# Performance work log

Hardware: AMD Instinct MI355X
Metric: run time of the kernel (lower is better)

## Reference

```python
import jax, jax.numpy as jnp
import numpy as np
from jax import lax

# Multi-scale VAR tokenizer encode: per scale, bilinear-resize the residual latent,
# FSQ-quantize it (Cosmos DI16x16 quantizer, levels [8,8,8,5,5,5]), then subtract the
# upsampled ResidualBlock(conv3x3 -> GELU -> conv3x3) reconstruction from the latent.

RESOLUTIONS = [(1, 1), (2, 2), (4, 4), (6, 6), (8, 8), (10, 10), (12, 12), (16, 16)]
LEVELS = np.array([8.0, 8.0, 8.0, 5.0, 5.0, 5.0], dtype=np.float32)  # FSQ levels, 6 channels
C, HIDDEN = 6, 48  # channels, channels * expansion_factor(8)
FSQ_EPS = 1e-3


def _resize(x, hw):
    # matches torch F.interpolate(mode='bilinear', align_corners=False) (half-pixel, no antialias)
    b, c = x.shape[0], x.shape[1]
    return jax.image.resize(x, (b, c, hw[0], hw[1]), method='bilinear', antialias=False)


def _fsq_quantize(z):
    # z: [B, 6, H, W] float32 -> codes in [-1, 1] quantized to per-channel levels
    l = jnp.asarray(LEVELS).reshape(1, C, 1, 1)
    half_l = (l - 1.0) * (1.0 + FSQ_EPS) / 2.0
    offset = jnp.where(jnp.mod(l, 2.0) == 0.0, 0.5, 0.0)
    shift = jnp.arctanh(offset / half_l)
    bounded = jnp.tanh(z + shift) * half_l - offset
    quantized = bounded + lax.stop_gradient(jnp.round(bounded) - bounded)  # straight-through
    half_width = jnp.floor(l / 2.0)
    return quantized / half_width


def _conv3x3(x, w, b):
    y = lax.conv_general_dilated(x, w, window_strides=(1, 1), padding='SAME',
                                 dimension_numbers=('NCHW', 'OIHW', 'NCHW'))
    return y + b.reshape(1, -1, 1, 1)


def _residual_block(x, w1, b1, w2, b2):
    h = _conv3x3(x, w1, b1)
    h = jax.nn.gelu(h, approximate=False)  # nn.GELU default = exact erf
    return _conv3x3(h, w2, b2)


def setup_inputs() -> dict:
    key = jax.random.key(0)
    k0, k1, k2 = jax.random.split(key, 3)
    B = 2048
    n = len(RESOLUTIONS)
    latents = jax.random.normal(k0, (B, C, 16, 16), dtype=jnp.float32)
    w1 = jax.random.normal(k1, (n, HIDDEN, C, 3, 3), dtype=jnp.float32) * 0.05
    b1 = jnp.zeros((n, HIDDEN), dtype=jnp.float32)
    w2 = jax.random.normal(k2, (n, C, HIDDEN, 3, 3), dtype=jnp.float32) * 0.05
    b2 = jnp.zeros((n, C), dtype=jnp.float32)
    return {"latents": latents, "w1": w1, "b1": b1, "w2": w2, "b2": b2}


def reference(latents, w1, b1, w2, b2):
    f = latents
    full_hw = f.shape[-2:]
    tokens = []
    for i, (h, w) in enumerate(RESOLUTIONS):
        f_curr = _resize(f, (h, w))
        r = _fsq_quantize(f_curr)  # tup[1] of Cosmos FSQ quantizer: quantized codes
        tokens.append(r)
        if i < len(RESOLUTIONS) - 1:
            z = _residual_block(r, w1[i], b1[i], w2[i], b2[i])
            z = _resize(z, full_hw)
            f = f - z
    # concatenate per-scale tokens flattened over (C,H,W) -> [B, 6*(1+4+16+36+64+100+144+256)] = [B, 3726]
    return jnp.concatenate([t.reshape(t.shape[0], -1) for t in tokens], axis=-1)
```

## Files before the change

### kernel.cpp

```cpp
#include <hip/hip_runtime.h>
#include <math.h>

#define NTHREADS 256

__constant__ int c_RESA[8] = {1, 2, 4, 6, 8, 10, 12, 16};
__constant__ int c_OFF6[8] = {0, 6, 30, 126, 342, 726, 1326, 2190};
__constant__ unsigned c_MAGIC[8] = {1048576u, 524288u, 262144u, 174763u,
                                    131072u, 104858u, 87382u, 65536u};

__global__ void __launch_bounds__(256)
prep_w2t_kernel(const float* __restrict__ w2g, float* __restrict__ w2t) {
    int tid = blockIdx.x * blockDim.x + threadIdx.x;
    for (int i = tid; i < 8 * 2592; i += gridDim.x * blockDim.x) {
        int e  = i & 3;
        int r  = i >> 2;
        int co = r % 6;  r /= 6;
        int c4 = r % 12; r /= 12;
        int j  = r % 9;
        int s  = r / 9;
        int ci = c4 * 4 + e;
        w2t[i] = w2g[((size_t)(s * 6 + co) * 48 + ci) * 9 + j];
    }
}

__device__ __forceinline__ void mk_tap(int o, float invs, int insz,
                                       int* i0, int* i1, float* w0, float* w1) {
    float fy = __fsub_rn(__fmul_rn(__fadd_rn((float)o, 0.5f), invs), 0.5f);
    float fl = floorf(fy);
    int y0 = (int)fl;
    float k0 = __fsub_rn(1.0f, fabsf(__fsub_rn(fy, fl)));
    float k1 = __fsub_rn(1.0f, fabsf(__fsub_rn(fy, __fadd_rn(fl, 1.0f))));
    bool v0 = (y0 >= 0);
    bool v1 = (y0 + 1 <= insz - 1);
    k0 = v0 ? k0 : 0.0f;
    k1 = v1 ? k1 : 0.0f;
    float ssum = __fadd_rn(k0, k1);
    *w0 = __fdiv_rn(k0, ssum);
    *w1 = __fdiv_rn(k1, ssum);
    *i0 = v0 ? y0 : 0;
    *i1 = v1 ? (y0 + 1) : (insz - 1);
}

__device__ __forceinline__ float gelu_exact(float x) {
    return __fmul_rn(__fmul_rn(0.5f, x),
                     __fadd_rn(1.0f, erff(__fmul_rn(x, 0.70710678118654752440f))));
}

__global__ void __launch_bounds__(NTHREADS)
var_tokenizer_kernel(const float* __restrict__ latents,
                     const float* __restrict__ w1g, const float* __restrict__ b1g,
                     const float* __restrict__ w2t, const float* __restrict__ b2g,
                     float* __restrict__ out) {
    __shared__ float f_l[1536];
    __shared__ float r_pad[6 * 196];
    __shared__ __align__(16) float h4[12 * 196 * 4];
    __shared__ float z_l[6 * 144];
    __shared__ int   dti0[16]; __shared__ int dti1[16];
    __shared__ float dtw0[16]; __shared__ float dtw1[16];
    __shared__ int   uti0[16]; __shared__ int uti1[16];
    __shared__ float utw0[16]; __shared__ float utw1[16];

    const int item = blockIdx.x;
    const int tid  = threadIdx.x;
    const int wv   = __builtin_amdgcn_readfirstlane(tid >> 6);
    const int lane = tid & 63;

    const float* lat  = latents + (size_t)item * 1536;
    float*       outb = out + (size_t)item * 3726;

    for (int i = tid; i < 1536; i += NTHREADS) f_l[i] = lat[i];
    for (int i = tid; i < 6 * 196;      i += NTHREADS) r_pad[i] = 0.0f;
    for (int i = tid; i < 12 * 196 * 4; i += NTHREADS) h4[i] = 0.0f;

    const float HL8 = (8.0f - 1.0f) * (1.0f + 1.0e-3f) / 2.0f;
    const float HL5 = (5.0f - 1.0f) * (1.0f + 1.0e-3f) / 2.0f;
    const float SH8 = (float)atanh((double)(0.5f / HL8));

    __syncthreads();

    for (int s = 0; s < 8; ++s) {
        const int R  = c_RESA[s];
        const int HW = R * R;
        const unsigned M = c_MAGIC[s];
        const bool last = (s == 7);

        if (tid < R) {
            float invs = __fdiv_rn(1.0f, __fdiv_rn((float)R, 16.0f));
            mk_tap(tid, invs, 16, &dti0[tid], &dti1[tid], &dtw0[tid], &dtw1[tid]);
        } else if (tid >= 64 && tid < 80 && !last) {
            int o = tid - 64;
            float invs = __fdiv_rn(1.0f, __fdiv_rn(16.0f, (float)R));
            mk_tap(o, invs, R, &uti0[o], &uti1[o], &utw0[o], &utw1[o]);
        }
        __syncthreads();

        const int off = c_OFF6[s];
        #pragma unroll 2
        for (int t = tid; t < 6 * HW; t += NTHREADS) {
            int rest = (int)(((unsigned)t * M) >> 20);
            int ox   = t - rest * R;
            int c    = (int)(((unsigned)rest * M) >> 20);
            int oy   = rest - c * R;
            float v;
            if (last) {
                v = f_l[t];
            } else {
                int y0 = dti0[oy], y1 = dti1[oy], x0 = dti0[ox], x1 = dti1[ox];
                float wy0 = dtw0[oy], wy1 = dtw1[oy], wx0 = dtw0[ox], wx1 = dtw1[ox];
                const float* fc = f_l + c * 256;
                float a00 = fc[y0 * 16 + x0], a01 = fc[y0 * 16 + x1];
                float a10 = fc[y1 * 16 + x0], a11 = fc[y1 * 16 + x1];
                float t0 = __fadd_rn(__fmul_rn(wy0, a00), __fmul_rn(wy1, a10));
                float t1 = __fadd_rn(__fmul_rn(wy0, a01), __fmul_rn(wy1, a11));
                v = __fadd_rn(__fmul_rn(wx0, t0), __fmul_rn(wx1, t1));
            }
            bool is8 = (c < 3);
            float hl   = is8 ? HL8 : HL5;
            float offc = is8 ? 0.5f : 0.0f;
            float sh   = is8 ? SH8 : 0.0f;
            float arg  = __fadd_rn(v, sh);
            float th32 = tanhf(arg);
            float b32  = __fsub_rn(__fmul_rn(th32, hl), offc);
            float r32  = rintf(b32);
            float d    = __fsub_rn(b32, r32);
            if (fabsf(fabsf(d) - 0.5f) < 1e-4f) {
                float th = (float)tanh((double)arg);
                r32 = rintf(__fsub_rn(__fmul_rn(th, hl), offc));
            }
            float q = __fmul_rn(r32, is8 ? 0.25f : 0.5f);
            outb[off + t] = q;
            if (!last) r_pad[c * 196 + (oy + 1) * 14 + (ox + 1)] = q;
        }
        if (last) break;
        __syncthreads();

        const float* w1s = w1g + (size_t)s * 2592;
        const float* b1s = b1g + (size_t)s * 48;
        for (int pb = 0; pb < HW; pb += 64) {
            int p = pb + lane;
            bool act = p < HW;
            int pc = act ? p : 0;
            int py = (int)(((unsigned)pc * M) >> 20);
            int px = pc - py * R;
            int pbase = py * 14 + px;
            int q = pbase + 15;
            float patch[6][9];
            #pragma unroll
            for (int ci = 0; ci < 6; ++ci) {
                const float* rp = r_pad + ci * 196 + pbase;
                #pragma unroll
                for (int dy = 0; dy < 3; ++dy) {
                    patch[ci][dy * 3 + 0] = rp[dy * 14 + 0];
                    patch[ci][dy * 3 + 1] = rp[dy * 14 + 1];
                    patch[ci][dy * 3 + 2] = rp[dy * 14 + 2];
                }
            }
            for (int g = 0; g < 3; ++g) {
                int kb = wv * 12 + g * 4;
                const float* wk0 = w1s + (kb + 0) * 54;
                const float* wk1 = w1s + (kb + 1) * 54;
                const float* wk2 = w1s + (kb + 2) * 54;
                const float* wk3 = w1s + (kb + 3) * 54;
                float a0 = 0.f, a1 = 0.f, a2 = 0.f, a3 = 0.f;
                #pragma unroll
                for (int ci = 0; ci < 6; ++ci)
                    #pragma unroll
                    for (int j = 0; j < 9; ++j) {
                        float pv = patch[ci][j];
                        int wi = ci * 9 + j;
                        a0 = __fmaf_rn(wk0[wi], pv, a0);
                        a1 = __fmaf_rn(wk1[wi], pv, a1);
                        a2 = __fmaf_rn(wk2[wi], pv, a2);
                        a3 = __fmaf_rn(wk3[wi], pv, a3);
                    }
                float4 hv;
                hv.x = gelu_exact(__fadd_rn(a0, b1s[kb + 0]));
                hv.y = gelu_exact(__fadd_rn(a1, b1s[kb + 1]));
                hv.z = gelu_exact(__fadd_rn(a2, b1s[kb + 2]));
                hv.w = gelu_exact(__fadd_rn(a3, b1s[kb + 3]));
                if (act) {
                    int c4u = wv * 3 + g;
                    *(float4*)&h4[(c4u * 196 + q) * 4] = hv;
                }
            }
        }
        __syncthreads();

        const float* w2sT = w2t + (size_t)s * 2592;
        const float* b2s  = b2g + (size_t)s * 6;
        {
            int p = tid;
            if (p < HW) {
                int py = (int)(((unsigned)p * M) >> 20);
                int px = p - py * R;
                float acc[6];
                #pragma unroll
                for (int co = 0; co < 6; ++co) acc[co] = 0.0f;
                for (int dy = 0; dy < 3; ++dy) {
                    for (int dx = 0; dx < 3; ++dx) {
                        int qq = (py + dy) * 14 + (px + dx);
                        const float* wjt = w2sT + (dy * 3 + dx) * 288;
                        #pragma unroll 2
                        for (int c4 = 0; c4 < 12; ++c4) {
                            float4 v = *(const float4*)&h4[(c4 * 196 + qq) * 4];
                            const float* wc = wjt + c4 * 24;
                            #pragma unroll
                            for (int co = 0; co < 6; ++co) {
                                acc[co] = __fmaf_rn(wc[co * 4 + 0], v.x, acc[co]);
                                acc[co] = __fmaf_rn(wc[co * 4 + 1], v.y, acc[co]);
                                acc[co] = __fmaf_rn(wc[co * 4 + 2], v.z, acc[co]);
                                acc[co] = __fmaf_rn(wc[co * 4 + 3], v.w, acc[co]);
                            }
                        }
                    }
                }
                #pragma unroll
                for (int co = 0; co < 6; ++co)
                    z_l[co * HW + p] = __fadd_rn(acc[co], b2s[co]);
            }
        }
        __syncthreads();

        for (int t = tid; t < 1536; t += NTHREADS) {
            int x = t & 15; int y = (t >> 4) & 15; int c = t >> 8;
            int y0 = uti0[y], y1 = uti1[y], x0 = uti0[x], x1 = uti1[x];
            float wy0 = utw0[y], wy1 = utw1[y], wx0 = utw0[x], wx1 = utw1[x];
            const float* zc = z_l + c * HW;
            float a00 = zc[y0 * R + x0], a01 = zc[y0 * R + x1];
            float a10 = zc[y1 * R + x0], a11 = zc[y1 * R + x1];
            float t0 = __fadd_rn(__fmul_rn(wy0, a00), __fmul_rn(wy1, a10));
            float t1 = __fadd_rn(__fmul_rn(wy0, a01), __fmul_rn(wy1, a11));
            float zv = __fadd_rn(__fmul_rn(wx0, t0), __fmul_rn(wx1, t1));
            f_l[t] = __fsub_rn(f_l[t], zv);
        }
        __syncthreads();
    }
}

extern "C" void kernel_launch(void* const* d_in, const int* in_sizes, int n_in,
                              void* d_out, int out_size, void* d_ws, size_t ws_size,
                              hipStream_t stream) {
    const float* latents = (const float*)d_in[0];
    const float* w1 = (const float*)d_in[1];
    const float* b1 = (const float*)d_in[2];
    const float* w2 = (const float*)d_in[3];
    const float* b2 = (const float*)d_in[4];
    float* out = (float*)d_out;
    float* w2t = (float*)d_ws;
    int nitems = in_sizes[0] / 1536;

    prep_w2t_kernel<<<40, 256, 0, stream>>>(w2, w2t);
    var_tokenizer_kernel<<<nitems, NTHREADS, 0, stream>>>(latents, w1, b1, w2t, b2, out);
}
```

Measured before the change: 793.8 us.

## Use packed v2 FMA for both convs with transposed weight layouts

Transposes the conv1 weights in the prep kernel so the four output channels of each group sit next to each other, and permutes the conv2 weights so output-channel pairs are adjacent. Both convolutions then accumulate through 2-wide vector FMAs, which can lower to packed fp32 FMA instructions on CDNA, roughly halving the FMA instruction count. Conv1 now handles all three channel groups of a wave in one pass over the patch instead of three separate loops. This needs more accumulator registers and a larger workspace, and the prep kernel now also transposes w1.

```diff
diff --git a/kernel.cpp b/kernel.cpp
--- a/kernel.cpp
+++ b/kernel.cpp
@@ -2,6 +2,15 @@
 #include <math.h>
 
 #define NTHREADS 256
+
+typedef float v2f __attribute__((ext_vector_type(2)));
+
+#if __has_builtin(__builtin_elementwise_fma)
+#define V2FMA(W, V, A) (A) = __builtin_elementwise_fma((W), (V), (A))
+#else
+#define V2FMA(W, V, A) do { (A).x = __fmaf_rn((W).x,(V).x,(A).x); \
+                            (A).y = __fmaf_rn((W).y,(V).y,(A).y); } while (0)
+#endif
 
 __constant__ int c_RESA[8] = {1, 2, 4, 6, 8, 10, 12, 16};
 __constant__ int c_OFF6[8] = {0, 6, 30, 126, 342, 726, 1326, 2190};
@@ -9,17 +18,26 @@
                                     131072u, 104858u, 87382u, 65536u};
 
 __global__ void __launch_bounds__(256)
-prep_w2t_kernel(const float* __restrict__ w2g, float* __restrict__ w2t) {
+prep_wt_kernel(const float* __restrict__ w1g, const float* __restrict__ w2g,
+               float* __restrict__ w1t, float* __restrict__ w2t) {
     int tid = blockIdx.x * blockDim.x + threadIdx.x;
-    for (int i = tid; i < 8 * 2592; i += gridDim.x * blockDim.x) {
-        int e  = i & 3;
+    int stride = gridDim.x * blockDim.x;
+    for (int i = tid; i < 8 * 2592; i += stride) {
+        int c  = i & 3;
         int r  = i >> 2;
-        int co = r % 6;  r /= 6;
+        int wi = r % 54; r /= 54;
+        int k4 = r % 12;
+        int s  = r / 12;
+        w1t[i] = w1g[(size_t)(s * 48 + k4 * 4 + c) * 54 + wi];
+    }
+    for (int i = tid; i < 8 * 2592; i += stride) {
+        int co = i % 6;
+        int r  = i / 6;
+        int e  = r & 3;  r >>= 2;
         int c4 = r % 12; r /= 12;
         int j  = r % 9;
         int s  = r / 9;
-        int ci = c4 * 4 + e;
-        w2t[i] = w2g[((size_t)(s * 6 + co) * 48 + ci) * 9 + j];
+        w2t[i] = w2g[((size_t)(s * 6 + co) * 48 + c4 * 4 + e) * 9 + j];
     }
 }
 
@@ -48,7 +66,7 @@
 
 __global__ void __launch_bounds__(NTHREADS)
 var_tokenizer_kernel(const float* __restrict__ latents,
-                     const float* __restrict__ w1g, const float* __restrict__ b1g,
+                     const float* __restrict__ w1t, const float* __restrict__ b1g,
                      const float* __restrict__ w2t, const float* __restrict__ b2g,
                      float* __restrict__ out) {
     __shared__ float f_l[1536];
@@ -134,8 +152,8 @@
         if (last) break;
         __syncthreads();
 
-        const float* w1s = w1g + (size_t)s * 2592;
-        const float* b1s = b1g + (size_t)s * 48;
+        const float* w1sT = w1t + (size_t)s * 2592;
+        const float* b1s  = b1g + (size_t)s * 48;
         for (int pb = 0; pb < HW; pb += 64) {
             int p = pb + lane;
             bool act = p < HW;
@@ -144,43 +162,61 @@
             int px = pc - py * R;
             int pbase = py * 14 + px;
             int q = pbase + 15;
-            float patch[6][9];
+            float patch[54];
             #pragma unroll
             for (int ci = 0; ci < 6; ++ci) {
                 const float* rp = r_pad + ci * 196 + pbase;
                 #pragma unroll
                 for (int dy = 0; dy < 3; ++dy) {
-                    patch[ci][dy * 3 + 0] = rp[dy * 14 + 0];
-                    patch[ci][dy * 3 + 1] = rp[dy * 14 + 1];
-                    patch[ci][dy * 3 + 2] = rp[dy * 14 + 2];
-                }
-            }
-            for (int g = 0; g < 3; ++g) {
-                int kb = wv * 12 + g * 4;
-                const float* wk0 = w1s + (kb + 0) * 54;
-                const float* wk1 = w1s + (kb + 1) * 54;
-                const float* wk2 = w1s + (kb + 2) * 54;
-                const float* wk3 = w1s + (kb + 3) * 54;
-                float a0 = 0.f, a1 = 0.f, a2 = 0.f, a3 = 0.f;
-                #pragma unroll
-                for (int ci = 0; ci < 6; ++ci)
-                    #pragma unroll
-                    for (int j = 0; j < 9; ++j) {
-                        float pv = patch[ci][j];
-                        int wi = ci * 9 + j;
-                        a0 = __fmaf_rn(wk0[wi], pv, a0);
-                        a1 = __fmaf_rn(wk1[wi], pv, a1);
-                        a2 = __fmaf_rn(wk2[wi], pv, a2);
-                        a3 = __fmaf_rn(wk3[wi], pv, a3);
-                    }
-                float4 hv;
-                hv.x = gelu_exact(__fadd_rn(a0, b1s[kb + 0]));
-                hv.y = gelu_exact(__fadd_rn(a1, b1s[kb + 1]));
-                hv.z = gelu_exact(__fadd_rn(a2, b1s[kb + 2]));
-                hv.w = gelu_exact(__fadd_rn(a3, b1s[kb + 3]));
-                if (act) {
-                    int c4u = wv * 3 + g;
-                    *(float4*)&h4[(c4u * 196 + q) * 4] = hv;
+                    patch[ci * 9 + dy * 3 + 0] = rp[dy * 14 + 0];
+                    patch[ci * 9 + dy * 3 + 1] = rp[dy * 14 + 1];
+                    patch[ci * 9 + dy * 3 + 2] = rp[dy * 14 + 2];
+                }
+            }
+            const float* wT0 = w1sT + (wv * 3 + 0) * 216;
+            const float* wT1 = w1sT + (wv * 3 + 1) * 216;
+            const float* wT2 = w1sT + (wv * 3 + 2) * 216;
+            v2f A0 = {0.f,0.f}, B0 = {0.f,0.f};
+            v2f A1 = {0.f,0.f}, B1 = {0.f,0.f};
+            v2f A2 = {0.f,0.f}, B2 = {0.f,0.f};
+            #pragma unroll
+            for (int wi = 0; wi < 54; ++wi) {
+                float pv = patch[wi];
+                v2f vv = {pv, pv};
+                V2FMA(((const v2f*)(wT0 + wi * 4))[0], vv, A0);
+                V2FMA(((const v2f*)(wT0 + wi * 4))[1], vv, B0);
+                V2FMA(((const v2f*)(wT1 + wi * 4))[0], vv, A1);
+                V2FMA(((const v2f*)(wT1 + wi * 4))[1], vv, B1);
+                V2FMA(((const v2f*)(wT2 + wi * 4))[0], vv, A2);
+                V2FMA(((const v2f*)(wT2 + wi * 4))[1], vv, B2);
+            }
+            if (act) {
+                {
+                    int kb = (wv * 3 + 0) * 4;
+                    float4 hv;
+                    hv.x = gelu_exact(__fadd_rn(A0.x, b1s[kb + 0]));
+                    hv.y = gelu_exact(__fadd_rn(A0.y, b1s[kb + 1]));
+                    hv.z = gelu_exact(__fadd_rn(B0.x, b1s[kb + 2]));
+                    hv.w = gelu_exact(__fadd_rn(B0.y, b1s[kb + 3]));
+                    *(float4*)&h4[((wv * 3 + 0) * 196 + q) * 4] = hv;
+                }
+                {
+                    int kb = (wv * 3 + 1) * 4;
+                    float4 hv;
+                    hv.x = gelu_exact(__fadd_rn(A1.x, b1s[kb + 0]));
+                    hv.y = gelu_exact(__fadd_rn(A1.y, b1s[kb + 1]));
+                    hv.z = gelu_exact(__fadd_rn(B1.x, b1s[kb + 2]));
+                    hv.w = gelu_exact(__fadd_rn(B1.y, b1s[kb + 3]));
+                    *(float4*)&h4[((wv * 3 + 1) * 196 + q) * 4] = hv;
+                }
+                {
+                    int kb = (wv * 3 + 2) * 4;
+                    float4 hv;
+                    hv.x = gelu_exact(__fadd_rn(A2.x, b1s[kb + 0]));
+                    hv.y = gelu_exact(__fadd_rn(A2.y, b1s[kb + 1]));
+                    hv.z = gelu_exact(__fadd_rn(B2.x, b1s[kb + 2]));
+                    hv.w = gelu_exact(__fadd_rn(B2.y, b1s[kb + 3]));
+                    *(float4*)&h4[((wv * 3 + 2) * 196 + q) * 4] = hv;
                 }
             }
         }
@@ -193,9 +229,7 @@
             if (p < HW) {
                 int py = (int)(((unsigned)p * M) >> 20);
                 int px = p - py * R;
-                float acc[6];
-                #pragma unroll
-                for (int co = 0; co < 6; ++co) acc[co] = 0.0f;
+                v2f a01 = {0.f,0.f}, a23 = {0.f,0.f}, a45 = {0.f,0.f};
                 for (int dy = 0; dy < 3; ++dy) {
                     for (int dx = 0; dx < 3; ++dx) {
                         int qq = (py + dy) * 14 + (px + dx);
@@ -203,20 +237,32 @@
                         #pragma unroll 2
                         for (int c4 = 0; c4 < 12; ++c4) {
                             float4 v = *(const float4*)&h4[(c4 * 196 + qq) * 4];
-                            const float* wc = wjt + c4 * 24;
-                            #pragma unroll
-                            for (int co = 0; co < 6; ++co) {
-                                acc[co] = __fmaf_rn(wc[co * 4 + 0], v.x, acc[co]);
-                                acc[co] = __fmaf_rn(wc[co * 4 + 1], v.y, acc[co]);
-                                acc[co] = __fmaf_rn(wc[co * 4 + 2], v.z, acc[co]);
-                                acc[co] = __fmaf_rn(wc[co * 4 + 3], v.w, acc[co]);
-                            }
+                            const v2f* wp = (const v2f*)(wjt + c4 * 24);
+                            v2f vx = {v.x, v.x};
+                            V2FMA(wp[0], vx, a01);
+                            V2FMA(wp[1], vx, a23);
+                            V2FMA(wp[2], vx, a45);
+                            v2f vy = {v.y, v.y};
+                            V2FMA(wp[3], vy, a01);
+                            V2FMA(wp[4], vy, a23);
+                            V2FMA(wp[5], vy, a45);
+                            v2f vz = {v.z, v.z};
+                            V2FMA(wp[6], vz, a01);
+                            V2FMA(wp[7], vz, a23);
+                            V2FMA(wp[8], vz, a45);
+                            v2f vw = {v.w, v.w};
+                            V2FMA(wp[9],  vw, a01);
+                            V2FMA(wp[10], vw, a23);
+                            V2FMA(wp[11], vw, a45);
                         }
                     }
                 }
-                #pragma unroll
-                for (int co = 0; co < 6; ++co)
-                    z_l[co * HW + p] = __fadd_rn(acc[co], b2s[co]);
+                z_l[0 * HW + p] = __fadd_rn(a01.x, b2s[0]);
+                z_l[1 * HW + p] = __fadd_rn(a01.y, b2s[1]);
+                z_l[2 * HW + p] = __fadd_rn(a23.x, b2s[2]);
+                z_l[3 * HW + p] = __fadd_rn(a23.y, b2s[3]);
+                z_l[4 * HW + p] = __fadd_rn(a45.x, b2s[4]);
+                z_l[5 * HW + p] = __fadd_rn(a45.y, b2s[5]);
             }
         }
         __syncthreads();
@@ -246,9 +292,10 @@
     const float* w2 = (const float*)d_in[3];
     const float* b2 = (const float*)d_in[4];
     float* out = (float*)d_out;
-    float* w2t = (float*)d_ws;
+    float* w1t = (float*)d_ws;
+    float* w2t = w1t + 8 * 2592;
     int nitems = in_sizes[0] / 1536;
 
-    prep_w2t_kernel<<<40, 256, 0, stream>>>(w2, w2t);
-    var_tokenizer_kernel<<<nitems, NTHREADS, 0, stream>>>(latents, w1, b1, w2t, b2, out);
-}
+    prep_wt_kernel<<<64, 256, 0, stream>>>(w1, w2, w1t, w2t);
+    var_tokenizer_kernel<<<nitems, NTHREADS, 0, stream>>>(latents, w1t, b1, w2t, b2, out);
+}
```

Result: slower. 938.7 us (+18.3%).
